# Kernel optimization log

Measured on AMD Instinct MI355X. Metric: run time of the kernel, lower is better.

## Reference

```python
import jax, jax.numpy as jnp
import numpy as np

C = 256
C8 = C // 8  # query/key channels
B, T, W, H = 4, 8, 32, 32


def setup_inputs() -> dict:
    key = jax.random.key(0)
    ks = jax.random.split(key, 8)
    s = 0.05
    return {
        "x": jax.random.normal(ks[0], (B, C, T, W, H), dtype=jnp.float32),
        "wq": jax.random.normal(ks[1], (C8, C), dtype=jnp.float32) * s,
        "bq": jax.random.normal(ks[2], (C8,), dtype=jnp.float32) * s,
        "wk": jax.random.normal(ks[3], (C8, C), dtype=jnp.float32) * s,
        "bk": jax.random.normal(ks[4], (C8,), dtype=jnp.float32) * s,
        "wv": jax.random.normal(ks[5], (C, C), dtype=jnp.float32) * s,
        "bv": jax.random.normal(ks[6], (C,), dtype=jnp.float32) * s,
        "gamma": jax.random.normal(ks[7], (1,), dtype=jnp.float32),
    }


def reference(x, wq, bq, wk, bk, wv, bv, gamma):
    b, c, t, w, h = x.shape
    n = w * h
    # Faithful to torch: x.view(-1, c, w, h) is a row-major reinterpretation
    xr = jnp.reshape(x, (-1, c, n))  # (m, C, N), m = B*T
    # 1x1 convs == per-pixel linear projections
    q = jnp.einsum("oc,mcn->mno", wq, xr) + bq            # (m, N, C8)
    k = jnp.einsum("oc,mcn->mon", wk, xr) + bk[:, None]   # (m, C8, N)
    v = jnp.einsum("oc,mcn->mon", wv, xr) + bv[:, None]   # (m, C, N)
    energy = jnp.einsum("mic,mcj->mij", q, k)             # (m, N, N), unscaled
    attention = jax.nn.softmax(energy, axis=-1)
    out = jnp.einsum("mcn,mnj->mcj", v, attention)        # V @ A (as in torch code)
    out = jnp.reshape(out, (b, c, t, w, h))
    return gamma * out + x
```

## Files before the change

### kernel.cpp

```cpp
#include <hip/hip_runtime.h>

#define MB    32
#define CCH   256
#define QCH   32
#define NPIX  1024
#define SLICE (CCH * NPIX)
#define L2E   1.44269504088896340736f
#define SHIFT 32.0f

typedef __bf16          bf16x8 __attribute__((ext_vector_type(8)));
typedef __bf16          bf16x4 __attribute__((ext_vector_type(4)));
typedef float           f32x4  __attribute__((ext_vector_type(4)));
typedef unsigned int    u32x4  __attribute__((ext_vector_type(4)));
typedef unsigned short  u16x4  __attribute__((ext_vector_type(4)));

__device__ __forceinline__ unsigned short f2bf(float f) {
    unsigned int u = __builtin_bit_cast(unsigned int, f);
    u += 0x7FFFu + ((u >> 16) & 1u);
    return (unsigned short)(u >> 16);
}
__device__ __forceinline__ u16x4 cvt4(float a, float b, float c, float d) {
    bf16x4 v = { (__bf16)a, (__bf16)b, (__bf16)c, (__bf16)d };
    return __builtin_bit_cast(u16x4, v);
}
__device__ __forceinline__ bf16x8 ldfrag(const unsigned short* p) {
    u32x4 u = *(const u32x4*)p;
    return __builtin_bit_cast(bf16x8, u);
}

#define WB_OFF 0u
#define A2_OFF 163840u
#define XT_OFF 294912u
#define QT_OFF 17072128u
#define KT_OFF 19169280u
#define V_OFF  21266432u

__global__ __launch_bounds__(256) void k_prep_w(
    const float* __restrict__ wq, const float* __restrict__ wk,
    const float* __restrict__ wv, unsigned short* __restrict__ Wb)
{
    int i4 = (blockIdx.x * 256 + threadIdx.x) * 4;
    int o = i4 >> 8, c = i4 & 255;
    const float* src = (o < 32) ? wq + (size_t)o * CCH + c
                     : (o < 64) ? wk + (size_t)(o - 32) * CCH + c
                                : wv + (size_t)(o - 64) * CCH + c;
    float4 v = *(const float4*)src;
    *(u16x4*)(Wb + i4) = cvt4(v.x, v.y, v.z, v.w);
}

__global__ __launch_bounds__(256) void k_prep_x(
    const float* __restrict__ x, unsigned short* __restrict__ Xt)
{
    __shared__ unsigned short Ts[64][72];
    const int t = threadIdx.x;
    const int n0 = blockIdx.x * 64, c0 = blockIdx.y * 64, mi = blockIdx.z;
    const float* xp = x + (size_t)mi * SLICE;
    unsigned short* Xp = Xt + (size_t)mi * SLICE;
#pragma unroll
    for (int r = 0; r < 4; ++r) {
        int cl = (t >> 4) + r * 16;
        int nl = (t & 15) * 4;
        float4 v = *(const float4*)(xp + (size_t)(c0 + cl) * NPIX + n0 + nl);
        Ts[nl + 0][cl] = f2bf(v.x); Ts[nl + 1][cl] = f2bf(v.y);
        Ts[nl + 2][cl] = f2bf(v.z); Ts[nl + 3][cl] = f2bf(v.w);
    }
    __syncthreads();
#pragma unroll
    for (int r = 0; r < 4; ++r) {
        int nl = (t >> 4) + r * 16;
        int cl = (t & 15) * 4;
        u16x4 d = *(const u16x4*)&Ts[nl][cl];
        *(u16x4*)(Xp + (size_t)(n0 + nl) * CCH + c0 + cl) = d;
    }
}

__global__ __launch_bounds__(256) void k_proj(
    const unsigned short* __restrict__ Wb, const unsigned short* __restrict__ Xt,
    const float* __restrict__ bq, const float* __restrict__ bk,
    const float* __restrict__ bv,
    unsigned short* __restrict__ Qt, unsigned short* __restrict__ Kt,
    unsigned short* __restrict__ V)
{
    __shared__ unsigned short Xs[64 * 268];

    const int t = threadIdx.x, lane = t & 63, w = t >> 6;
    const int lj = lane & 15, q = lane >> 4;
    const int n0 = blockIdx.x * 64;
    const int mi = blockIdx.y;
    const unsigned short* Xp = Xt + (size_t)mi * SLICE;

#pragma unroll
    for (int r = 0; r < 8; ++r) {
        int idx = t + r * 256;
        int row = idx >> 5, seg = idx & 31;
        u32x4 d = *(const u32x4*)(Xp + (size_t)(n0 + row) * CCH + seg * 8);
        *(u32x4*)&Xs[row * 268 + seg * 8] = d;
    }
    __syncthreads();

    f32x4 acc[5][4];
#pragma unroll
    for (int i = 0; i < 5; ++i)
#pragma unroll
        for (int b = 0; b < 4; ++b) acc[i][b] = (f32x4){0.f, 0.f, 0.f, 0.f};

    const unsigned short* wbase = Wb + (size_t)(w * 16 + lj) * CCH + q * 8;
    const unsigned short* xbase = &Xs[lj * 268 + q * 8];

#pragma unroll 2
    for (int kc = 0; kc < CCH; kc += 32) {
        bf16x8 a[5];
#pragma unroll
        for (int i = 0; i < 5; ++i)
            a[i] = ldfrag(wbase + (size_t)i * 64 * CCH + kc);
        bf16x8 xb[4];
#pragma unroll
        for (int b = 0; b < 4; ++b)
            xb[b] = ldfrag(xbase + b * 16 * 268 + kc);
#pragma unroll
        for (int i = 0; i < 5; ++i)
#pragma unroll
            for (int b = 0; b < 4; ++b)
                acc[i][b] = __builtin_amdgcn_mfma_f32_16x16x32_bf16(a[i], xb[b], acc[i][b], 0, 0, 0);
    }

#pragma unroll
    for (int i = 0; i < 5; ++i) {
        const int o16 = (w + 4 * i) * 16;
        const int ob = o16 + 4 * q;
        if (o16 < 32) {
            unsigned short* Qp = Qt + (size_t)mi * NPIX * QCH;
            float b0 = bq[ob], b1 = bq[ob + 1], b2 = bq[ob + 2], b3 = bq[ob + 3];
#pragma unroll
            for (int b = 0; b < 4; ++b) {
                int n = n0 + b * 16 + lj;
                *(u16x4*)(Qp + (size_t)n * QCH + ob) =
                    cvt4((acc[i][b][0] + b0) * L2E, (acc[i][b][1] + b1) * L2E,
                         (acc[i][b][2] + b2) * L2E, (acc[i][b][3] + b3) * L2E);
            }
        } else if (o16 < 64) {
            unsigned short* Kp = Kt + (size_t)mi * NPIX * QCH;
            int o2 = ob - 32;
            float b0 = bk[o2], b1 = bk[o2 + 1], b2 = bk[o2 + 2], b3 = bk[o2 + 3];
#pragma unroll
            for (int b = 0; b < 4; ++b) {
                int n = n0 + b * 16 + lj;
                *(u16x4*)(Kp + (size_t)n * QCH + o2) =
                    cvt4(acc[i][b][0] + b0, acc[i][b][1] + b1,
                         acc[i][b][2] + b2, acc[i][b][3] + b3);
            }
        } else {
            unsigned short* Vw = V + (size_t)mi * SLICE;
            const int c16 = (o16 - 64) >> 4;
            const int n05 = n0 >> 5;
            const int cb = (o16 - 64) + 4 * q;
            float bb[4] = { bv[cb], bv[cb + 1], bv[cb + 2], bv[cb + 3] };
            const int ni = lj & 7;
#pragma unroll
            for (int b = 0; b < 4; ++b) {
                int n5 = n05 + (b >> 1);
                int fl = ((2 * b + (lj >> 3)) & 3) * 16 + 4 * q;
                size_t base = ((size_t)(c16 * 32 + n5) * 64 + fl) * 8 + ni;
#pragma unroll
                for (int r = 0; r < 4; ++r)
                    Vw[base + (size_t)r * 8] = f2bf(acc[i][b][r] + bb[r]);
            }
        }
    }
}

__global__ __launch_bounds__(256) void k_stats(
    const unsigned short* __restrict__ Qt, const unsigned short* __restrict__ Kt,
    float* __restrict__ a2f)
{
    const int t = threadIdx.x, lane = t & 63, w = t >> 6;
    const int lj = lane & 15, q = lane >> 4;
    const int n16 = blockIdx.x * 64 + w * 16;
    const int mi = blockIdx.y;
    const unsigned short* Qp = Qt + (size_t)mi * NPIX * QCH;
    const unsigned short* Kp = Kt + (size_t)mi * NPIX * QCH;

    bf16x8 qa = ldfrag(Qp + (size_t)(n16 + lj) * QCH + q * 8);

    float s[4] = { 0.f, 0.f, 0.f, 0.f };
#pragma unroll 8
    for (int jc = 0; jc < NPIX; jc += 16) {
        bf16x8 kb = ldfrag(Kp + (size_t)(jc + lj) * QCH + q * 8);
        f32x4 z = (f32x4){0.f, 0.f, 0.f, 0.f};
        f32x4 e = __builtin_amdgcn_mfma_f32_16x16x32_bf16(qa, kb, z, 0, 0, 0);
#pragma unroll
        for (int r = 0; r < 4; ++r) s[r] += exp2f(e[r] - SHIFT);
    }
#pragma unroll
    for (int msk = 1; msk <= 8; msk <<= 1)
#pragma unroll
        for (int r = 0; r < 4; ++r) s[r] += __shfl_xor(s[r], msk, 64);

    if (lj == 0) {
        float* apo = a2f + (size_t)mi * NPIX;
#pragma unroll
        for (int r = 0; r < 4; ++r)
            apo[n16 + 4 * q + r] = SHIFT + log2f(s[r]);
    }
}

__global__ __launch_bounds__(256) void k_attn_out(
    const float* __restrict__ x, const float* __restrict__ gamma,
    const unsigned short* __restrict__ Qt, const unsigned short* __restrict__ Kt,
    const unsigned short* __restrict__ Vf, const float* __restrict__ a2f,
    float* __restrict__ out)
{
    __shared__ unsigned short Vs[2][8 * 512];
    __shared__ unsigned short Ps[4][32][36];

    const int b = blockIdx.x;
    const int mi  = (b & 7) | ((b >> 7) << 3);
    const int sub = (b >> 3) & 15;
    const int j0  = (sub & 7) * 128;
    const int cb  = sub >> 3;

    const int t = threadIdx.x, lane = t & 63, w = t >> 6;
    const int lj = lane & 15, q = lane >> 4;
    const int jw = j0 + w * 32;

    const unsigned short* Qp = Qt + (size_t)mi * NPIX * QCH;
    const unsigned short* Kp = Kt + (size_t)mi * NPIX * QCH;
    const unsigned short* Vp = Vf + (size_t)mi * SLICE;
    const float* ap = a2f + (size_t)mi * NPIX;

    bf16x8 kb[2];
#pragma unroll
    for (int sj = 0; sj < 2; ++sj)
        kb[sj] = ldfrag(Kp + (size_t)(jw + sj * 16 + lj) * QCH + q * 8);

    const int ctl = t >> 5, ln0 = (t & 31) * 2;
    const unsigned short* vsrc0 = Vp + ((size_t)(cb * 8 + ctl) * 32) * 512 + ln0 * 8;

    f32x4 acc[8][2];
#pragma unroll
    for (int ci = 0; ci < 8; ++ci)
#pragma unroll
        for (int ji = 0; ji < 2; ++ji) acc[ci][ji] = (f32x4){0.f, 0.f, 0.f, 0.f};

    {
        u32x4 d0 = *(const u32x4*)vsrc0;
        u32x4 d1 = *(const u32x4*)(vsrc0 + 8);
        *(u32x4*)&Vs[0][ctl * 512 + ln0 * 8] = d0;
        *(u32x4*)&Vs[0][ctl * 512 + ln0 * 8 + 8] = d1;
    }
    bf16x8 qa_n[2];
    f32x4  a4_n[2];
#pragma unroll
    for (int sn = 0; sn < 2; ++sn) {
        qa_n[sn] = ldfrag(Qp + (size_t)(sn * 16 + lj) * QCH + q * 8);
        a4_n[sn] = *(const f32x4*)(ap + sn * 16 + 4 * q);
    }
    __syncthreads();

    int p = 0;
    for (int nc = 0; nc < NPIX; nc += 32, p ^= 1) {
        const int nn = (nc + 32) & (NPIX - 1);
        const unsigned short* vsrc = vsrc0 + (size_t)(nn >> 5) * 512;
        u32x4 nv0 = *(const u32x4*)vsrc;
        u32x4 nv1 = *(const u32x4*)(vsrc + 8);

        bf16x8 qa0 = qa_n[0], qa1 = qa_n[1];
        f32x4 a40 = a4_n[0], a41 = a4_n[1];
#pragma unroll
        for (int sj = 0; sj < 2; ++sj) {
            f32x4 z = (f32x4){0.f, 0.f, 0.f, 0.f};
            f32x4 e0 = __builtin_amdgcn_mfma_f32_16x16x32_bf16(qa0, kb[sj], z, 0, 0, 0);
            f32x4 e1 = __builtin_amdgcn_mfma_f32_16x16x32_bf16(qa1, kb[sj], z, 0, 0, 0);
            *(u16x4*)&Ps[w][sj * 16 + lj][4 * q] =
                cvt4(exp2f(e0[0] - a40[0]), exp2f(e0[1] - a40[1]),
                     exp2f(e0[2] - a40[2]), exp2f(e0[3] - a40[3]));
            *(u16x4*)&Ps[w][sj * 16 + lj][16 + 4 * q] =
                cvt4(exp2f(e1[0] - a41[0]), exp2f(e1[1] - a41[1]),
                     exp2f(e1[2] - a41[2]), exp2f(e1[3] - a41[3]));
        }
#pragma unroll
        for (int sn = 0; sn < 2; ++sn) {
            qa_n[sn] = ldfrag(Qp + (size_t)(nn + sn * 16 + lj) * QCH + q * 8);
            a4_n[sn] = *(const f32x4*)(ap + nn + sn * 16 + 4 * q);
        }

        bf16x8 pf[2];
#pragma unroll
        for (int ji = 0; ji < 2; ++ji)
            pf[ji] = ldfrag(&Ps[w][ji * 16 + lj][q * 8]);
#pragma unroll
        for (int ci = 0; ci < 8; ++ci) {
            bf16x8 vfr = ldfrag(&Vs[p][ci * 512 + lane * 8]);
#pragma unroll
            for (int ji = 0; ji < 2; ++ji)
                acc[ci][ji] = __builtin_amdgcn_mfma_f32_16x16x32_bf16(vfr, pf[ji], acc[ci][ji], 0, 0, 0);
        }

        *(u32x4*)&Vs[p ^ 1][ctl * 512 + ln0 * 8] = nv0;
        *(u32x4*)&Vs[p ^ 1][ctl * 512 + ln0 * 8 + 8] = nv1;
        __syncthreads();
    }

    const float g = gamma[0];
    const size_t obase = (size_t)mi * SLICE;
#pragma unroll
    for (int ci = 0; ci < 8; ++ci) {
#pragma unroll
        for (int ji = 0; ji < 2; ++ji) {
#pragma unroll
            for (int r = 0; r < 4; ++r) {
                int c = cb * 128 + ci * 16 + 4 * q + r;
                int j = jw + ji * 16 + lj;
                size_t off = obase + (size_t)c * NPIX + j;
                out[off] = g * acc[ci][ji][r] + x[off];
            }
        }
    }
}

extern "C" void kernel_launch(void* const* d_in, const int* in_sizes, int n_in,
                              void* d_out, int out_size, void* d_ws, size_t ws_size,
                              hipStream_t stream)
{
    const float* x     = (const float*)d_in[0];
    const float* wq    = (const float*)d_in[1];
    const float* bq    = (const float*)d_in[2];
    const float* wk    = (const float*)d_in[3];
    const float* bk    = (const float*)d_in[4];
    const float* wv    = (const float*)d_in[5];
    const float* bv    = (const float*)d_in[6];
    const float* gamma = (const float*)d_in[7];
    float* out = (float*)d_out;

    char* wsb = (char*)d_ws;
    unsigned short* Wb = (unsigned short*)(wsb + WB_OFF);
    float*          a2 = (float*)(wsb + A2_OFF);
    unsigned short* Xt = (unsigned short*)(wsb + XT_OFF);
    unsigned short* Qt = (unsigned short*)(wsb + QT_OFF);
    unsigned short* Kt = (unsigned short*)(wsb + KT_OFF);
    unsigned short* V  = (unsigned short*)(wsb + V_OFF);

    k_prep_w<<<80, 256, 0, stream>>>(wq, wk, wv, Wb);
    k_prep_x<<<dim3(NPIX / 64, CCH / 64, MB), 256, 0, stream>>>(x, Xt);
    k_proj<<<dim3(NPIX / 64, MB), 256, 0, stream>>>(Wb, Xt, bq, bk, bv, Qt, Kt, V);
    k_stats<<<dim3(NPIX / 64, MB), 256, 0, stream>>>(Qt, Kt, a2);
    k_attn_out<<<512, 256, 0, stream>>>(x, gamma, Qt, Kt, V, a2, out);
}
```

Before: 182.2 us.

## Fuse x transpose into projection and materialize unnormalized attention matrix

Removes the separate x-to-bf16 transpose kernel by converting and transposing x inside the projection kernel. Adds a path that computes exp scores once in the stats pass, writes the unnormalized P matrix to workspace in MFMA fragment layout, and folds the softmax normalization into V by scaling each V column by its reciprocal row sum. The output kernel then becomes a plain V·P GEMM without recomputing QK^T and exp. This trades recomputation for a large extra write and read of a 64MB bf16 matrix and depends on the workspace being big enough, falling back to the old path otherwise.

Result: faster. 168.5 us (-7.5%).

```diff
diff --git a/kernel.cpp b/kernel.cpp
--- a/kernel.cpp
+++ b/kernel.cpp
@@ -23,17 +23,22 @@
     bf16x4 v = { (__bf16)a, (__bf16)b, (__bf16)c, (__bf16)d };
     return __builtin_bit_cast(u16x4, v);
 }
+__device__ __forceinline__ float bf2f(unsigned short u) {
+    unsigned int v = (unsigned int)u << 16;
+    return __builtin_bit_cast(float, v);
+}
 __device__ __forceinline__ bf16x8 ldfrag(const unsigned short* p) {
     u32x4 u = *(const u32x4*)p;
     return __builtin_bit_cast(bf16x8, u);
 }
 
-#define WB_OFF 0u
-#define A2_OFF 163840u
-#define XT_OFF 294912u
-#define QT_OFF 17072128u
-#define KT_OFF 19169280u
-#define V_OFF  21266432u
+#define WB_OFF  0u
+#define QT_OFF  262144u
+#define KT_OFF  2359296u
+#define V_OFF   4456448u
+#define A2F_OFF 21233664u
+#define PU_OFF  21364736u
+#define WS_NEED 88473600u
 
 __global__ __launch_bounds__(256) void k_prep_w(
     const float* __restrict__ wq, const float* __restrict__ wk,
@@ -48,34 +53,8 @@
     *(u16x4*)(Wb + i4) = cvt4(v.x, v.y, v.z, v.w);
 }
 
-__global__ __launch_bounds__(256) void k_prep_x(
-    const float* __restrict__ x, unsigned short* __restrict__ Xt)
-{
-    __shared__ unsigned short Ts[64][72];
-    const int t = threadIdx.x;
-    const int n0 = blockIdx.x * 64, c0 = blockIdx.y * 64, mi = blockIdx.z;
-    const float* xp = x + (size_t)mi * SLICE;
-    unsigned short* Xp = Xt + (size_t)mi * SLICE;
-#pragma unroll
-    for (int r = 0; r < 4; ++r) {
-        int cl = (t >> 4) + r * 16;
-        int nl = (t & 15) * 4;
-        float4 v = *(const float4*)(xp + (size_t)(c0 + cl) * NPIX + n0 + nl);
-        Ts[nl + 0][cl] = f2bf(v.x); Ts[nl + 1][cl] = f2bf(v.y);
-        Ts[nl + 2][cl] = f2bf(v.z); Ts[nl + 3][cl] = f2bf(v.w);
-    }
-    __syncthreads();
-#pragma unroll
-    for (int r = 0; r < 4; ++r) {
-        int nl = (t >> 4) + r * 16;
-        int cl = (t & 15) * 4;
-        u16x4 d = *(const u16x4*)&Ts[nl][cl];
-        *(u16x4*)(Xp + (size_t)(n0 + nl) * CCH + c0 + cl) = d;
-    }
-}
-
 __global__ __launch_bounds__(256) void k_proj(
-    const unsigned short* __restrict__ Wb, const unsigned short* __restrict__ Xt,
+    const float* __restrict__ x, const unsigned short* __restrict__ Wb,
     const float* __restrict__ bq, const float* __restrict__ bk,
     const float* __restrict__ bv,
     unsigned short* __restrict__ Qt, unsigned short* __restrict__ Kt,
@@ -87,14 +66,22 @@
     const int lj = lane & 15, q = lane >> 4;
     const int n0 = blockIdx.x * 64;
     const int mi = blockIdx.y;
-    const unsigned short* Xp = Xt + (size_t)mi * SLICE;
+    const float* xp = x + (size_t)mi * SLICE;
 
 #pragma unroll
     for (int r = 0; r < 8; ++r) {
-        int idx = t + r * 256;
-        int row = idx >> 5, seg = idx & 31;
-        u32x4 d = *(const u32x4*)(Xp + (size_t)(n0 + row) * CCH + seg * 8);
-        *(u32x4*)&Xs[row * 268 + seg * 8] = d;
+        int job = t + r * 256;
+        int cp = job >> 4;
+        int seg = job & 15;
+        float4 va = *(const float4*)(xp + (size_t)(2 * cp) * NPIX + n0 + seg * 4);
+        float4 vb = *(const float4*)(xp + (size_t)(2 * cp + 1) * NPIX + n0 + seg * 4);
+        u16x4 da = cvt4(va.x, va.y, va.z, va.w);
+        u16x4 db = cvt4(vb.x, vb.y, vb.z, vb.w);
+#pragma unroll
+        for (int e = 0; e < 4; ++e) {
+            unsigned pk = (unsigned)da[e] | ((unsigned)db[e] << 16);
+            *(unsigned*)&Xs[(seg * 4 + e) * 268 + 2 * cp] = pk;
+        }
     }
     __syncthreads();
 
@@ -169,6 +156,172 @@
     }
 }
 
+__global__ __launch_bounds__(256) void k_stats_pu(
+    const unsigned short* __restrict__ Qt, const unsigned short* __restrict__ Kt,
+    unsigned short* __restrict__ V, unsigned short* __restrict__ Pu)
+{
+    __shared__ unsigned short Ps[4][32][36];
+    __shared__ float rs[128];
+
+    const int t = threadIdx.x, lane = t & 63, w = t >> 6;
+    const int lj = lane & 15, q = lane >> 4;
+    const int n0b = blockIdx.x * 128;
+    const int nw = n0b + w * 32;
+    const int mi = blockIdx.y;
+    const unsigned short* Qp = Qt + (size_t)mi * NPIX * QCH;
+    const unsigned short* Kp = Kt + (size_t)mi * NPIX * QCH;
+    unsigned short* Pup = Pu + (size_t)mi * NPIX * NPIX;
+
+    bf16x8 qa[2];
+#pragma unroll
+    for (int h = 0; h < 2; ++h)
+        qa[h] = ldfrag(Qp + (size_t)(nw + h * 16 + lj) * QCH + q * 8);
+
+    float s[2][4];
+#pragma unroll
+    for (int h = 0; h < 2; ++h)
+#pragma unroll
+        for (int r = 0; r < 4; ++r) s[h][r] = 0.f;
+
+#pragma unroll 2
+    for (int jc = 0; jc < NPIX; jc += 32) {
+#pragma unroll
+        for (int f = 0; f < 2; ++f) {
+            bf16x8 kb = ldfrag(Kp + (size_t)(jc + f * 16 + lj) * QCH + q * 8);
+#pragma unroll
+            for (int h = 0; h < 2; ++h) {
+                f32x4 z = (f32x4){0.f, 0.f, 0.f, 0.f};
+                f32x4 e = __builtin_amdgcn_mfma_f32_16x16x32_bf16(qa[h], kb, z, 0, 0, 0);
+                float p0 = exp2f(e[0] - SHIFT), p1 = exp2f(e[1] - SHIFT);
+                float p2 = exp2f(e[2] - SHIFT), p3 = exp2f(e[3] - SHIFT);
+                s[h][0] += p0; s[h][1] += p1; s[h][2] += p2; s[h][3] += p3;
+                *(u16x4*)&Ps[w][f * 16 + lj][h * 16 + 4 * q] = cvt4(p0, p1, p2, p3);
+            }
+        }
+#pragma unroll
+        for (int f = 0; f < 2; ++f) {
+            u32x4 bfrag = *(const u32x4*)&Ps[w][f * 16 + lj][q * 8];
+            *(u32x4*)(Pup + ((size_t)((jc >> 4) + f) * 32 + (nw >> 5)) * 512 + lane * 8) = bfrag;
+        }
+    }
+
+#pragma unroll
+    for (int msk = 1; msk <= 8; msk <<= 1)
+#pragma unroll
+        for (int h = 0; h < 2; ++h)
+#pragma unroll
+            for (int r = 0; r < 4; ++r) s[h][r] += __shfl_xor(s[h][r], msk, 64);
+    if (lj == 0) {
+#pragma unroll
+        for (int h = 0; h < 2; ++h)
+#pragma unroll
+            for (int r = 0; r < 4; ++r)
+                rs[w * 32 + h * 16 + 4 * q + r] = 1.0f / s[h][r];
+    }
+    __syncthreads();
+
+    unsigned short* Vp = V + (size_t)mi * SLICE;
+    const int n5b = n0b >> 5;
+#pragma unroll
+    for (int r = 0; r < 16; ++r) {
+        int job = t + r * 256;
+        int fr = job >> 6, ln = job & 63;
+        size_t base = ((size_t)((fr >> 2) * 32 + n5b + (fr & 3)) * 64 + ln) * 8;
+        u16x4 lo = *(const u16x4*)(Vp + base);
+        u16x4 hi = *(const u16x4*)(Vp + base + 4);
+        const float* rp = &rs[(fr & 3) * 32 + (ln >> 4) * 8];
+        u16x4 nlo = cvt4(bf2f(lo[0]) * rp[0], bf2f(lo[1]) * rp[1],
+                         bf2f(lo[2]) * rp[2], bf2f(lo[3]) * rp[3]);
+        u16x4 nhi = cvt4(bf2f(hi[0]) * rp[4], bf2f(hi[1]) * rp[5],
+                         bf2f(hi[2]) * rp[6], bf2f(hi[3]) * rp[7]);
+        *(u16x4*)(Vp + base) = nlo;
+        *(u16x4*)(Vp + base + 4) = nhi;
+    }
+}
+
+__global__ __launch_bounds__(256) void k_gemm_out(
+    const float* __restrict__ x, const float* __restrict__ gamma,
+    const unsigned short* __restrict__ Vf, const unsigned short* __restrict__ Pu,
+    float* __restrict__ out)
+{
+    __shared__ unsigned short Vs[2][8 * 512];
+
+    const int b = blockIdx.x;
+    const int mi  = (b & 7) | ((b >> 7) << 3);
+    const int sub = (b >> 3) & 15;
+    const int j0  = (sub & 7) * 128;
+    const int cb  = sub >> 3;
+
+    const int t = threadIdx.x, lane = t & 63, w = t >> 6;
+    const int lj = lane & 15, q = lane >> 4;
+    const int jw = j0 + w * 32;
+
+    const unsigned short* Vp  = Vf + (size_t)mi * SLICE;
+    const unsigned short* Pup = Pu + (size_t)mi * NPIX * NPIX
+                              + ((size_t)(jw >> 4) * 32) * 512 + lane * 8;
+
+    const int ctl = t >> 5, ln0 = (t & 31) * 2;
+    const unsigned short* vsrc0 = Vp + ((size_t)(cb * 8 + ctl) * 32) * 512 + ln0 * 8;
+
+    f32x4 acc[8][2];
+#pragma unroll
+    for (int ci = 0; ci < 8; ++ci)
+#pragma unroll
+        for (int f = 0; f < 2; ++f) acc[ci][f] = (f32x4){0.f, 0.f, 0.f, 0.f};
+
+    {
+        u32x4 d0 = *(const u32x4*)vsrc0;
+        u32x4 d1 = *(const u32x4*)(vsrc0 + 8);
+        *(u32x4*)&Vs[0][ctl * 512 + ln0 * 8] = d0;
+        *(u32x4*)&Vs[0][ctl * 512 + ln0 * 8 + 8] = d1;
+    }
+    bf16x8 pf[2];
+#pragma unroll
+    for (int f = 0; f < 2; ++f) pf[f] = ldfrag(Pup + f * 16384);
+    __syncthreads();
+
+    int p = 0;
+    for (int nc = 0; nc < NPIX; nc += 32, p ^= 1) {
+        const int nn = (nc + 32) & (NPIX - 1);
+        const unsigned short* vsrc = vsrc0 + (size_t)(nn >> 5) * 512;
+        u32x4 nv0 = *(const u32x4*)vsrc;
+        u32x4 nv1 = *(const u32x4*)(vsrc + 8);
+        bf16x8 pf_n[2];
+#pragma unroll
+        for (int f = 0; f < 2; ++f)
+            pf_n[f] = ldfrag(Pup + f * 16384 + (size_t)(nn >> 5) * 512);
+
+#pragma unroll
+        for (int ci = 0; ci < 8; ++ci) {
+            bf16x8 vfr = ldfrag(&Vs[p][ci * 512 + lane * 8]);
+#pragma unroll
+            for (int f = 0; f < 2; ++f)
+                acc[ci][f] = __builtin_amdgcn_mfma_f32_16x16x32_bf16(vfr, pf[f], acc[ci][f], 0, 0, 0);
+        }
+
+        *(u32x4*)&Vs[p ^ 1][ctl * 512 + ln0 * 8] = nv0;
+        *(u32x4*)&Vs[p ^ 1][ctl * 512 + ln0 * 8 + 8] = nv1;
+        __syncthreads();
+        pf[0] = pf_n[0]; pf[1] = pf_n[1];
+    }
+
+    const float g = gamma[0];
+    const size_t obase = (size_t)mi * SLICE;
+#pragma unroll
+    for (int ci = 0; ci < 8; ++ci) {
+#pragma unroll
+        for (int f = 0; f < 2; ++f) {
+#pragma unroll
+            for (int r = 0; r < 4; ++r) {
+                int c = cb * 128 + ci * 16 + 4 * q + r;
+                int j = jw + f * 16 + lj;
+                size_t off = obase + (size_t)c * NPIX + j;
+                out[off] = g * acc[ci][f][r] + x[off];
+            }
+        }
+    }
+}
+
 __global__ __launch_bounds__(256) void k_stats(
     const unsigned short* __restrict__ Qt, const unsigned short* __restrict__ Kt,
     float* __restrict__ a2f)
@@ -195,7 +348,6 @@
     for (int msk = 1; msk <= 8; msk <<= 1)
 #pragma unroll
         for (int r = 0; r < 4; ++r) s[r] += __shfl_xor(s[r], msk, 64);
-
     if (lj == 0) {
         float* apo = a2f + (size_t)mi * NPIX;
 #pragma unroll
@@ -334,15 +486,20 @@
 
     char* wsb = (char*)d_ws;
     unsigned short* Wb = (unsigned short*)(wsb + WB_OFF);
-    float*          a2 = (float*)(wsb + A2_OFF);
-    unsigned short* Xt = (unsigned short*)(wsb + XT_OFF);
     unsigned short* Qt = (unsigned short*)(wsb + QT_OFF);
     unsigned short* Kt = (unsigned short*)(wsb + KT_OFF);
     unsigned short* V  = (unsigned short*)(wsb + V_OFF);
+    float*          a2 = (float*)(wsb + A2F_OFF);
+    unsigned short* Pu = (unsigned short*)(wsb + PU_OFF);
 
     k_prep_w<<<80, 256, 0, stream>>>(wq, wk, wv, Wb);
-    k_prep_x<<<dim3(NPIX / 64, CCH / 64, MB), 256, 0, stream>>>(x, Xt);
-    k_proj<<<dim3(NPIX / 64, MB), 256, 0, stream>>>(Wb, Xt, bq, bk, bv, Qt, Kt, V);
-    k_stats<<<dim3(NPIX / 64, MB), 256, 0, stream>>>(Qt, Kt, a2);
-    k_attn_out<<<512, 256, 0, stream>>>(x, gamma, Qt, Kt, V, a2, out);
-}
+    k_proj<<<dim3(NPIX / 64, MB), 256, 0, stream>>>(x, Wb, bq, bk, bv, Qt, Kt, V);
+
+    if (ws_size >= (size_t)WS_NEED) {
+        k_stats_pu<<<dim3(NPIX / 128, MB), 256, 0, stream>>>(Qt, Kt, V, Pu);
+        k_gemm_out<<<512, 256, 0, stream>>>(x, gamma, V, Pu, out);
+    } else {
+        k_stats<<<dim3(NPIX / 64, MB), 256, 0, stream>>>(Qt, Kt, a2);
+        k_attn_out<<<512, 256, 0, stream>>>(x, gamma, Qt, Kt, V, a2, out);
+    }
+}
```
